# Kernel tuning notes

Hardware: AMD Instinct MI355X
Metric: run time of the kernel (lower is better)

Reference implementation:

```python
import jax, jax.numpy as jnp
import numpy as np

# Module hyperparameters (init_kwargs)
KH, KW = 1, 1            # kernel_size
PATCH_H, PATCH_W = 21, 21  # patch_size (displacement grid)
SH, SW = 1, 1            # stride
PAD_H, PAD_W = 0, 0      # padding
DILP_H, DILP_W = 1, 1    # dilation_patch
B, C, H, W = 8, 256, 64, 96


def setup_inputs() -> dict:
    key = jax.random.key(0)
    k1, k2 = jax.random.split(key)
    input1 = jax.random.normal(k1, (B, C, H, W), dtype=jnp.float32)
    input2 = jax.random.normal(k2, (B, C, H, W), dtype=jnp.float32)
    return {"input1": input1, "input2": input2}


def _correlation(x1, x2):
    """FlowNet-style spatial correlation (cost volume).

    out[b, pi, pj, i, j] = sum_{c, ki, kj}
        x1_pad[b, c, i*SH + ki, j*SW + kj] *
        x2_pad[b, c, i*SH + ki + (pi - radH)*DILP_H, j*SW + kj + (pj - radW)*DILP_W]
    Out-of-bounds reads of x2 are zero (handled by padding).
    """
    radH, radW = PATCH_H // 2, PATCH_W // 2
    x1p = jnp.pad(x1, ((0, 0), (0, 0), (PAD_H, PAD_H), (PAD_W, PAD_W)))
    x2p = jnp.pad(x2, ((0, 0), (0, 0),
                       (PAD_H + radH * DILP_H, PAD_H + radH * DILP_H),
                       (PAD_W + radW * DILP_W, PAD_W + radW * DILP_W)))
    Hp, Wp = H + 2 * PAD_H, W + 2 * PAD_W
    oH = (Hp - KH) // SH + 1
    oW = (Wp - KW) // SW + 1

    # displacement grid -> start offsets into x2p (0 corresponds to -rad shift)
    sh = jnp.arange(PATCH_H, dtype=jnp.int32) * DILP_H
    sw = jnp.arange(PATCH_W, dtype=jnp.int32) * DILP_W
    starts = jnp.stack(jnp.meshgrid(sh, sw, indexing="ij"), axis=-1).reshape(-1, 2)

    def step(carry, s):
        # shifted view of x2 aligned with padded x1
        sl = jax.lax.dynamic_slice(x2p, (0, 0, s[0], s[1]), (B, C, Hp, Wp))
        prod = jnp.sum(x1p * sl, axis=1)  # [B, Hp, Wp], channel reduction
        # kernel-window sum + output stride (KH=KW=1 -> single strided slice)
        acc = jnp.zeros((B, oH, oW), dtype=prod.dtype)
        for ki in range(KH):
            for kj in range(KW):
                acc = acc + jax.lax.slice(
                    prod, (0, ki, kj),
                    (B, ki + (oH - 1) * SH + 1, kj + (oW - 1) * SW + 1),
                    (1, SH, SW))
        return carry, acc

    _, out = jax.lax.scan(step, None, starts)  # [PATCH_H*PATCH_W, B, oH, oW]
    out = out.reshape(PATCH_H, PATCH_W, B, oH, oW)
    return jnp.transpose(out, (2, 0, 1, 3, 4))  # [B, patchH, patchW, oH, oW]


def reference(input1, input2):
    return _correlation(input1, input2)
```

## Files before the change

kernel.cpp:

```cpp
#include <hip/hip_runtime.h>

typedef __attribute__((ext_vector_type(8))) short short8;
typedef __attribute__((ext_vector_type(4))) float f32x4;
typedef __attribute__((ext_vector_type(4))) unsigned short us4;

constexpr int NB = 8, NC = 256, IH = 64, IW = 96;
constexpr int PATCH = 21, RAD = 10;
constexpr int TI = 8, TJ = 8;
constexpr int WIN = 28, NWIN = 784;
constexpr int KC = 32, NKS = NC / KC;
constexpr int PLANE = IH * IW;
constexpr int PH = IH + 2 * RAD, PW = IW + 2 * RAD;
constexpr int WCH = 448;
constexpr int WBUF = 8 * WCH;
constexpr int ASTR = IH * IW * KC;
constexpr int BSTR = PH * PW * KC;
constexpr size_t X1T_ELEMS = (size_t)NB * NKS * ASTR;
constexpr size_t X2P_ELEMS = (size_t)NB * NKS * BSTR;
constexpr int GSTR = 65;
constexpr int X1BLKS = NB * IH * 8;
constexpr int X2BLKS = NB * PH * 8;

__device__ __forceinline__ unsigned short f2bf(float f) {
  unsigned u = __builtin_bit_cast(unsigned, f);
  u += 0x7fffu + ((u >> 16) & 1u);
  return (unsigned short)(u >> 16);
}

__global__ __launch_bounds__(256) void prepass_kmajor(
    const float* __restrict__ x1, const float* __restrict__ x2,
    unsigned short* __restrict__ x1k, unsigned short* __restrict__ x2k) {
  __shared__ float lsf[32 * 97];
  const int t = threadIdx.x;
  if (blockIdx.x < X1BLKS) {
    const int blk = blockIdx.x;
    const int ct = blk & 7, i = (blk >> 3) & 63, b = blk >> 9;
    const int c0 = ct * 32;
    const float* sp = x1 + ((size_t)b * NC + c0) * PLANE + (size_t)i * IW;
#pragma unroll
    for (int k = 0; k < 3; ++k) {
      int idx = k * 256 + t;
      int c = idx / 24, j4 = idx - c * 24;
      f32x4 v = *(const f32x4*)(sp + (size_t)c * PLANE + 4 * j4);
      float* lp = &lsf[c * 97 + 4 * j4];
      lp[0] = v[0]; lp[1] = v[1]; lp[2] = v[2]; lp[3] = v[3];
    }
    __syncthreads();
    unsigned short* dp = x1k + (((size_t)(b * NKS + ct) * IH + i) * IW) * KC;
#pragma unroll
    for (int k = 0; k < 3; ++k) {
      int o = k * 256 + t;
      int j = o >> 3, cq = o & 7;
      us4 v = {f2bf(lsf[(cq * 4 + 0) * 97 + j]), f2bf(lsf[(cq * 4 + 1) * 97 + j]),
               f2bf(lsf[(cq * 4 + 2) * 97 + j]), f2bf(lsf[(cq * 4 + 3) * 97 + j])};
      *(us4*)&dp[(size_t)j * KC + cq * 4] = v;
    }
  } else {
    const int blk = blockIdx.x - X1BLKS;
    const int ct = blk & 7, i = (blk >> 3) % PH, b = blk / (PH * 8);
    const int c0 = ct * 32;
    const int isrc = i - RAD;
    const bool rowok = (unsigned)isrc < (unsigned)IH;
    if (rowok) {
      const float* sp = x2 + ((size_t)b * NC + c0) * PLANE + (size_t)isrc * IW;
#pragma unroll
      for (int k = 0; k < 3; ++k) {
        int idx = k * 256 + t;
        int c = idx / 24, j4 = idx - c * 24;
        f32x4 v = *(const f32x4*)(sp + (size_t)c * PLANE + 4 * j4);
        float* lp = &lsf[c * 97 + 4 * j4];
        lp[0] = v[0]; lp[1] = v[1]; lp[2] = v[2]; lp[3] = v[3];
      }
    }
    __syncthreads();
    unsigned short* dp = x2k + (((size_t)(b * NKS + ct) * PH + i) * PW) * KC;
#pragma unroll
    for (int k = 0; k < 4; ++k) {
      int o = k * 256 + t;
      if (o < PW * 8) {
        int j = o >> 3, cq = o & 7;
        int jsrc = j - RAD;
        us4 v = {0, 0, 0, 0};
        if (rowok && (unsigned)jsrc < (unsigned)IW)
          v = us4{f2bf(lsf[(cq * 4 + 0) * 97 + jsrc]), f2bf(lsf[(cq * 4 + 1) * 97 + jsrc]),
                  f2bf(lsf[(cq * 4 + 2) * 97 + jsrc]), f2bf(lsf[(cq * 4 + 3) * 97 + jsrc])};
        *(us4*)&dp[(size_t)j * KC + cq * 4] = v;
      }
    }
  }
}

__global__ __launch_bounds__(512, 2) void corr_wavepipe(
    const unsigned short* __restrict__ x1k, const unsigned short* __restrict__ x2k,
    float* __restrict__ out) {
  __shared__ __attribute__((aligned(16))) unsigned short ls[2 * WBUF * 8];

  const int t = threadIdx.x, lane = t & 63, wv = t >> 6;
  const int bid = blockIdx.x;
  const int b = bid & 7;
  const int tile = bid >> 3;
  const int ti = tile / 12, tj = tile - ti * 12;
  const int i0 = ti * TI, j0 = tj * TJ;
  const int cbeg = 6 * wv;
  const int qk = lane >> 4, lr = lane & 15;

  const unsigned short* x1b = x1k + (size_t)b * NKS * ASTR;
  const unsigned short* x2b = x2k + (size_t)b * NKS * BSTR;

  const unsigned short* srcp[7];
#pragma unroll
  for (int s = 0; s < 7; ++s) {
    int c = s * 64 + lane;
    int w = ((c >> 3) << 1) | (((c >> 2) ^ (c >> 4)) & 1);
    int c4 = (c & 3) ^ (w & 3);
    int n = 96 * wv + w;
    int wi = n / WIN, wj = n - wi * WIN;
    srcp[s] = x2b + ((size_t)(i0 + wi) * PW + (j0 + wj)) * KC + c4 * 8;
  }
  const unsigned short* srcA =
      x1b + ((size_t)(i0 + (lr >> 3)) * IW + (j0 + (lr & 7))) * KC + qk * 8;
  constexpr size_t AOFF = (size_t)2 * IW * KC;

  f32x4 acc[4][7];
#pragma unroll
  for (int a = 0; a < 4; ++a)
#pragma unroll
    for (int cc = 0; cc < 7; ++cc) acc[a][cc] = (f32x4){0.f, 0.f, 0.f, 0.f};

  short8 aA0, aA1, aA2, aA3, aB0, aB1, aB2, aB3;

#define ALOAD(S, KS)                                                                \
  {                                                                                 \
    const unsigned short* ap = srcA + (size_t)(KS) * ASTR;                          \
    a##S##0 = *(const short8*)(ap);                                                 \
    a##S##1 = *(const short8*)(ap + AOFF);                                          \
    a##S##2 = *(const short8*)(ap + 2 * AOFF);                                      \
    a##S##3 = *(const short8*)(ap + 3 * AOFF);                                      \
  }

#define STAGEW(BUF, KS)                                                             \
  {                                                                                 \
    unsigned short* lb = &ls[((BUF) * WBUF + wv * WCH) * 8];                        \
    _Pragma("unroll")                                                               \
    for (int s = 0; s < 7; ++s)                                                     \
      __builtin_amdgcn_global_load_lds(                                             \
          (const void*)(srcp[s] + (size_t)(KS) * BSTR),                             \
          (void*)(lb + s * 512), 16, 0, 0);                                         \
  }

#define COMPUTE(BUF, S)                                                             \
  {                                                                                 \
    const unsigned short* lb = &ls[((BUF) * WBUF + wv * WCH) * 8];                  \
    _Pragma("unroll")                                                               \
    for (int cc = 0; cc < 7; ++cc) {                                                \
      int wl = 16 * cc + lr;                                                        \
      int slot = (4 * wl + qk) ^ (lr & 7);                                          \
      short8 bf = *(const short8*)(lb + slot * 8);                                  \
      acc[0][cc] = __builtin_amdgcn_mfma_f32_16x16x32_bf16(a##S##0, bf, acc[0][cc], 0, 0, 0); \
      acc[1][cc] = __builtin_amdgcn_mfma_f32_16x16x32_bf16(a##S##1, bf, acc[1][cc], 0, 0, 0); \
      acc[2][cc] = __builtin_amdgcn_mfma_f32_16x16x32_bf16(a##S##2, bf, acc[2][cc], 0, 0, 0); \
      acc[3][cc] = __builtin_amdgcn_mfma_f32_16x16x32_bf16(a##S##3, bf, acc[3][cc], 0, 0, 0); \
    }                                                                               \
  }

  ALOAD(A, 0)
  STAGEW(0, 0)
  asm volatile("" ::: "memory");
  ALOAD(B, 1)
  STAGEW(1, 1)

#define ITER(KS, SL, SC, VM)                                                        \
  if ((KS) >= 1 && (KS) < 7) { ALOAD(SL, (KS) + 1) STAGEW(((KS) + 1) & 1, (KS) + 1) } \
  asm volatile("s_waitcnt vmcnt(" #VM ")" ::: "memory");                            \
  COMPUTE((KS) & 1, SC)

  ITER(0, A, A, 11)
  ITER(1, A, B, 11)
  ITER(2, B, A, 11)
  ITER(3, A, B, 11)
  ITER(4, B, A, 11)
  ITER(5, A, B, 11)
  ITER(6, B, A, 11)
  ITER(7, A, B, 0)
#undef ITER
#undef COMPUTE
#undef STAGEW
#undef ALOAD

  float* gf = (float*)ls;
#pragma unroll
  for (int ch = 0; ch < 2; ++ch) {
    __syncthreads();
    const int n0 = ch ? 384 : 0;
#pragma unroll
    for (int a = 0; a < 4; ++a)
#pragma unroll
      for (int cc = 0; cc < 7; ++cc) {
        int ccg = cbeg + cc;
        if (ch ? (ccg >= 24) : (ccg <= 24)) {
          int nl = 16 * ccg + lr - n0;
          int mb = 16 * a + 4 * qk;
          float* gp = &gf[nl * GSTR + mb];
          gp[0] = acc[a][cc][0]; gp[1] = acc[a][cc][1];
          gp[2] = acc[a][cc][2]; gp[3] = acc[a][cc][3];
        }
      }
    __syncthreads();
    for (int s = t; s < 1764; s += 512) {
      int pidx = s / 21, pj = s - pidx * 21;
      int ii = 0, rem = pidx, stop = 0;
#pragma unroll
      for (int k = 0; k < 7; ++k) {
        int cnt = ch ? (7 + k) : (14 - k);
        int go = (!stop) && (rem >= cnt);
        rem -= go ? cnt : 0;
        ii += go;
        stop |= !go;
      }
      int pi = ch ? (14 - ii + rem) : rem;
      int nl = 28 * (pi + ii) + pj - n0;
      int ms = 8 * ii;
      float g[8];
#pragma unroll
      for (int e = 0; e < 8; ++e) g[e] = gf[(nl + e) * GSTR + ms + e];
      float* op = out + ((((size_t)b * PATCH + pi) * PATCH + pj) * IH + (i0 + ii)) * IW + j0;
      f32x4 v0 = {g[0], g[1], g[2], g[3]};
      f32x4 v1 = {g[4], g[5], g[6], g[7]};
      *(f32x4*)op = v0;
      *(f32x4*)(op + 4) = v1;
    }
  }
}

constexpr int LDKF = 40;
__global__ __launch_bounds__(512, 2) void corr_mfma_fb(
    const float* __restrict__ x1, const float* __restrict__ x2, float* __restrict__ out) {
  __shared__ __attribute__((aligned(16))) unsigned short lsA[64 * LDKF];
  __shared__ __attribute__((aligned(16))) unsigned short lsB[NWIN * LDKF];
  const int t = threadIdx.x;
  const int b = blockIdx.y;
  const int ti = blockIdx.x / 12, tj = blockIdx.x % 12;
  const int i0 = ti * TI, j0 = tj * TJ;
  const int lane = t & 63, wv = t >> 6;
  const int mtp = wv >> 2, cg = wv & 3, cbeg = cg * 12;
  const int qk = lane >> 4, lr = lane & 15;
  f32x4 acc[2][13];
#pragma unroll
  for (int a = 0; a < 2; ++a)
#pragma unroll
    for (int cc = 0; cc < 13; ++cc) acc[a][cc] = (f32x4){0.f, 0.f, 0.f, 0.f};
  const int am = t & 63, ak4 = t >> 6;
  const int aii = am >> 3, ajj = am & 7;
  const float* x1p = x1 + ((size_t)b * NC + 4 * ak4) * PLANE + (size_t)(i0 + aii) * IW + (j0 + ajj);
  const float* x2b = x2 + (size_t)b * NC * PLANE;
  for (int ks = 0; ks < NKS; ++ks) {
    __syncthreads();
    {
      const float* p = x1p + (size_t)ks * KC * PLANE;
      us4 v = {f2bf(p[0]), f2bf(p[PLANE]), f2bf(p[2 * PLANE]), f2bf(p[3 * PLANE])};
      *(us4*)&lsA[am * LDKF + 4 * ak4] = v;
    }
    for (int w = t; w < NWIN; w += 512) {
      const int wi = w / WIN, wj = w - wi * WIN;
      const int gi = i0 - RAD + wi, gj = j0 - RAD + wj;
      const bool ok = ((unsigned)gi < (unsigned)IH) && ((unsigned)gj < (unsigned)IW);
      const float* p = x2b + ((size_t)(ks * KC) * IH + gi) * IW + gj;
      unsigned short* dst = &lsB[w * LDKF];
#pragma unroll
      for (int k4 = 0; k4 < 8; ++k4) {
        const float* q = p + (size_t)(4 * k4) * PLANE;
        us4 v = {f2bf(ok ? q[0] : 0.f), f2bf(ok ? q[PLANE] : 0.f),
                 f2bf(ok ? q[2 * PLANE] : 0.f), f2bf(ok ? q[3 * PLANE] : 0.f)};
        *(us4*)&dst[4 * k4] = v;
      }
    }
    __syncthreads();
    short8 a0 = *(const short8*)&lsA[(32 * mtp + lr) * LDKF + 8 * qk];
    short8 a1 = *(const short8*)&lsA[(32 * mtp + 16 + lr) * LDKF + 8 * qk];
#pragma unroll
    for (int cc = 0; cc < 13; ++cc) {
      const int wrow = 16 * (cbeg + cc) + lr;
      short8 bf = *(const short8*)&lsB[wrow * LDKF + 8 * qk];
      acc[0][cc] = __builtin_amdgcn_mfma_f32_16x16x32_bf16(a0, bf, acc[0][cc], 0, 0, 0);
      acc[1][cc] = __builtin_amdgcn_mfma_f32_16x16x32_bf16(a1, bf, acc[1][cc], 0, 0, 0);
    }
  }
#pragma unroll
  for (int a = 0; a < 2; ++a) {
    const int mb = 16 * (2 * mtp + a) + qk * 4;
#pragma unroll
    for (int cc = 0; cc < 13; ++cc) {
      if (cg > 0 && cc == 0) continue;
      const int n = 16 * (cbeg + cc) + lr;
      const int wi = n / WIN, wj = n - wi * WIN;
#pragma unroll
      for (int r = 0; r < 4; ++r) {
        const int m = mb + r;
        const int ii = m >> 3, jj = m & 7;
        const int pi = wi - ii, pj = wj - jj;
        if ((unsigned)pi < (unsigned)PATCH && (unsigned)pj < (unsigned)PATCH)
          out[((((size_t)b * PATCH + pi) * PATCH + pj) * IH + (i0 + ii)) * IW + (j0 + jj)] =
              acc[a][cc][r];
      }
    }
  }
}

extern "C" void kernel_launch(void* const* d_in, const int* in_sizes, int n_in,
                              void* d_out, int out_size, void* d_ws, size_t ws_size,
                              hipStream_t stream) {
  const float* x1 = (const float*)d_in[0];
  const float* x2 = (const float*)d_in[1];
  float* out = (float*)d_out;
  const size_t need = (X1T_ELEMS + X2P_ELEMS) * sizeof(unsigned short);
  if (ws_size >= need) {
    unsigned short* x1k = (unsigned short*)d_ws;
    unsigned short* x2k = x1k + X1T_ELEMS;
    prepass_kmajor<<<X1BLKS + X2BLKS, 256, 0, stream>>>(x1, x2, x1k, x2k);
    corr_wavepipe<<<NB * 96, 512, 0, stream>>>(x1k, x2k, out);
  } else {
    dim3 grid(96, NB);
    corr_mfma_fb<<<grid, 512, 0, stream>>>(x1, x2, out);
  }
}
```

Measured before the change: 85.64 us.

## Triple-buffer x2 window staging and drop redundant overlapping column tiles

```diff
diff --git a/kernel.cpp b/kernel.cpp
--- a/kernel.cpp
+++ b/kernel.cpp
@@ -11,8 +11,7 @@
 constexpr int KC = 32, NKS = NC / KC;
 constexpr int PLANE = IH * IW;
 constexpr int PH = IH + 2 * RAD, PW = IW + 2 * RAD;
-constexpr int WCH = 448;
-constexpr int WBUF = 8 * WCH;
+constexpr int NCHB = 3136;
 constexpr int ASTR = IH * IW * KC;
 constexpr int BSTR = PH * PW * KC;
 constexpr size_t X1T_ELEMS = (size_t)NB * NKS * ASTR;
@@ -90,10 +89,10 @@
   }
 }
 
-__global__ __launch_bounds__(512, 2) void corr_wavepipe(
+__global__ __launch_bounds__(512, 2) void corr_wavepipe2(
     const unsigned short* __restrict__ x1k, const unsigned short* __restrict__ x2k,
     float* __restrict__ out) {
-  __shared__ __attribute__((aligned(16))) unsigned short ls[2 * WBUF * 8];
+  __shared__ __attribute__((aligned(16))) unsigned short ls[3 * NCHB * 8];
 
   const int t = threadIdx.x, lane = t & 63, wv = t >> 6;
   const int bid = blockIdx.x;
@@ -102,7 +101,9 @@
   const int ti = tile / 12, tj = tile - ti * 12;
   const int i0 = ti * TI, j0 = tj * TJ;
   const int cbeg = 6 * wv;
+  const int nt = (wv == 7) ? 7 : 6;
   const int qk = lane >> 4, lr = lane & 15;
+  const int woff = 384 * wv;
 
   const unsigned short* x1b = x1k + (size_t)b * NKS * ASTR;
   const unsigned short* x2b = x2k + (size_t)b * NKS * BSTR;
@@ -114,6 +115,7 @@
     int w = ((c >> 3) << 1) | (((c >> 2) ^ (c >> 4)) & 1);
     int c4 = (c & 3) ^ (w & 3);
     int n = 96 * wv + w;
+    if (n > 783) n = 783;
     int wi = n / WIN, wj = n - wi * WIN;
     srcp[s] = x2b + ((size_t)(i0 + wi) * PW + (j0 + wj)) * KC + c4 * 8;
   }
@@ -127,7 +129,7 @@
 #pragma unroll
     for (int cc = 0; cc < 7; ++cc) acc[a][cc] = (f32x4){0.f, 0.f, 0.f, 0.f};
 
-  short8 aA0, aA1, aA2, aA3, aB0, aB1, aB2, aB3;
+  short8 aA0, aA1, aA2, aA3, aB0, aB1, aB2, aB3, aC0, aC1, aC2, aC3;
 
 #define ALOAD(S, KS)                                                                \
   {                                                                                 \
@@ -140,26 +142,32 @@
 
 #define STAGEW(BUF, KS)                                                             \
   {                                                                                 \
-    unsigned short* lb = &ls[((BUF) * WBUF + wv * WCH) * 8];                        \
+    unsigned short* lb = &ls[((BUF) * NCHB + woff) * 8];                            \
     _Pragma("unroll")                                                               \
-    for (int s = 0; s < 7; ++s)                                                     \
+    for (int s = 0; s < 6; ++s)                                                     \
       __builtin_amdgcn_global_load_lds(                                             \
           (const void*)(srcp[s] + (size_t)(KS) * BSTR),                             \
           (void*)(lb + s * 512), 16, 0, 0);                                         \
+    if (wv == 7)                                                                    \
+      __builtin_amdgcn_global_load_lds(                                             \
+          (const void*)(srcp[6] + (size_t)(KS) * BSTR),                             \
+          (void*)(lb + 6 * 512), 16, 0, 0);                                         \
   }
 
 #define COMPUTE(BUF, S)                                                             \
   {                                                                                 \
-    const unsigned short* lb = &ls[((BUF) * WBUF + wv * WCH) * 8];                  \
+    const unsigned short* lb = &ls[((BUF) * NCHB + woff) * 8];                      \
     _Pragma("unroll")                                                               \
     for (int cc = 0; cc < 7; ++cc) {                                                \
-      int wl = 16 * cc + lr;                                                        \
-      int slot = (4 * wl + qk) ^ (lr & 7);                                          \
-      short8 bf = *(const short8*)(lb + slot * 8);                                  \
-      acc[0][cc] = __builtin_amdgcn_mfma_f32_16x16x32_bf16(a##S##0, bf, acc[0][cc], 0, 0, 0); \
-      acc[1][cc] = __builtin_amdgcn_mfma_f32_16x16x32_bf16(a##S##1, bf, acc[1][cc], 0, 0, 0); \
-      acc[2][cc] = __builtin_amdgcn_mfma_f32_16x16x32_bf16(a##S##2, bf, acc[2][cc], 0, 0, 0); \
-      acc[3][cc] = __builtin_amdgcn_mfma_f32_16x16x32_bf16(a##S##3, bf, acc[3][cc], 0, 0, 0); \
+      if (cc < nt) {                                                                \
+        int wl = 16 * cc + lr;                                                      \
+        int slot = (4 * wl + qk) ^ (lr & 7);                                        \
+        short8 bf = *(const short8*)(lb + slot * 8);                                \
+        acc[0][cc] = __builtin_amdgcn_mfma_f32_16x16x32_bf16(a##S##0, bf, acc[0][cc], 0, 0, 0); \
+        acc[1][cc] = __builtin_amdgcn_mfma_f32_16x16x32_bf16(a##S##1, bf, acc[1][cc], 0, 0, 0); \
+        acc[2][cc] = __builtin_amdgcn_mfma_f32_16x16x32_bf16(a##S##2, bf, acc[2][cc], 0, 0, 0); \
+        acc[3][cc] = __builtin_amdgcn_mfma_f32_16x16x32_bf16(a##S##3, bf, acc[3][cc], 0, 0, 0); \
+      }                                                                             \
     }                                                                               \
   }
 
@@ -168,20 +176,24 @@
   asm volatile("" ::: "memory");
   ALOAD(B, 1)
   STAGEW(1, 1)
-
-#define ITER(KS, SL, SC, VM)                                                        \
-  if ((KS) >= 1 && (KS) < 7) { ALOAD(SL, (KS) + 1) STAGEW(((KS) + 1) & 1, (KS) + 1) } \
-  asm volatile("s_waitcnt vmcnt(" #VM ")" ::: "memory");                            \
-  COMPUTE((KS) & 1, SC)
-
-  ITER(0, A, A, 11)
-  ITER(1, A, B, 11)
-  ITER(2, B, A, 11)
-  ITER(3, A, B, 11)
-  ITER(4, B, A, 11)
-  ITER(5, A, B, 11)
-  ITER(6, B, A, 11)
-  ITER(7, A, B, 0)
+  asm volatile("" ::: "memory");
+  ALOAD(C, 2)
+  STAGEW(2, 2)
+
+#define ITER(KS, SL, SC, VMA, VMB)                                                  \
+  if ((KS) < 6) { ALOAD(SL, (KS) + 2) STAGEW(((KS) + 2) % 3, (KS) + 2) }            \
+  if (wv == 7) { asm volatile("s_waitcnt vmcnt(" #VMB ")" ::: "memory"); }          \
+  else         { asm volatile("s_waitcnt vmcnt(" #VMA ")" ::: "memory"); }          \
+  COMPUTE((KS) % 3, SC)
+
+  ITER(0, C, A, 20, 22)
+  ITER(1, A, B, 20, 22)
+  ITER(2, B, C, 20, 22)
+  ITER(3, C, A, 20, 22)
+  ITER(4, A, B, 20, 22)
+  ITER(5, B, C, 20, 22)
+  ITER(6, C, A, 10, 11)
+  ITER(7, C, B, 0, 0)
 #undef ITER
 #undef COMPUTE
 #undef STAGEW
@@ -197,7 +209,7 @@
 #pragma unroll
       for (int cc = 0; cc < 7; ++cc) {
         int ccg = cbeg + cc;
-        if (ch ? (ccg >= 24) : (ccg <= 24)) {
+        if (cc < nt && (ch ? (ccg >= 24) : (ccg <= 24))) {
           int nl = 16 * ccg + lr - n0;
           int mb = 16 * a + 4 * qk;
           float* gp = &gf[nl * GSTR + mb];
@@ -317,7 +329,7 @@
     unsigned short* x1k = (unsigned short*)d_ws;
     unsigned short* x2k = x1k + X1T_ELEMS;
     prepass_kmajor<<<X1BLKS + X2BLKS, 256, 0, stream>>>(x1, x2, x1k, x2k);
-    corr_wavepipe<<<NB * 96, 512, 0, stream>>>(x1k, x2k, out);
+    corr_wavepipe2<<<NB * 96, 512, 0, stream>>>(x1k, x2k, out);
   } else {
     dim3 grid(96, NB);
     corr_mfma_fb<<<grid, 512, 0, stream>>>(x1, x2, out);
```

New measurement: 87.49 us. 1.02x slower.
